# Kernel tuning notes

Measured on AMD Instinct MI355X. Metric: run time of the kernel, lower is better.

The kernel has to match this reference:

```python
import jax, jax.numpy as jnp
import numpy as np

D_MODEL = 256
N_LEVELS = 4
N_HEADS = 8
N_POINTS = 4
LEN_Q = 1024
LEN_X = 256
SHAPES_NP = np.array([[100, 100], [50, 50], [25, 25], [13, 13]], dtype=np.int32)
LEN_IN = int((SHAPES_NP[:, 0] * SHAPES_NP[:, 1]).sum())  # 13294


def setup_inputs() -> dict:
    key = jax.random.key(0)
    ks = jax.random.split(key, 10)
    s = 0.02
    lvl_start = np.concatenate([[0], np.cumsum(SHAPES_NP[:, 0] * SHAPES_NP[:, 1])[:-1]]).astype(np.int32)
    return {
        "query": jax.random.normal(ks[0], (1, LEN_Q, D_MODEL), jnp.float32),
        "reference_points": jax.random.uniform(ks[1], (1, LEN_Q, N_LEVELS, 2), jnp.float32),
        "input_flatten": jax.random.normal(ks[2], (1, LEN_IN, D_MODEL), jnp.float32),
        "input_spatial_shapes": jnp.asarray(SHAPES_NP, jnp.int32),
        "add_keys": jax.random.normal(ks[3], (1, LEN_X, D_MODEL), jnp.float32),
        "input_level_start_index": jnp.asarray(lvl_start, jnp.int32),
        "W_off": jax.random.normal(ks[4], (N_HEADS * N_LEVELS * N_POINTS * 2, D_MODEL), jnp.float32) * s,
        "b_off": jax.random.normal(ks[5], (N_HEADS * N_LEVELS * N_POINTS * 2,), jnp.float32),
        "W_attn": jax.random.normal(ks[6], (N_HEADS * (N_LEVELS + 1), D_MODEL, D_MODEL), jnp.float32) * s,
        "W_val": jax.random.normal(ks[7], (2 * N_HEADS, D_MODEL, D_MODEL), jnp.float32) * s,
        "b_val": jax.random.normal(ks[8], (2 * N_HEADS, D_MODEL), jnp.float32) * s,
        "W_mix": jax.random.normal(ks[9], (D_MODEL, N_HEADS + 1), jnp.float32) * s,
    }


def reference(query, reference_points, input_flatten, input_spatial_shapes, add_keys,
              input_level_start_index, W_off, b_off, W_attn, W_val, b_val, W_mix):
    N, Lq, C = query.shape
    H, L, P = N_HEADS, N_LEVELS, N_POINTS

    # sampling offsets: (N, Lq, H, L, P, 2)
    off = (query @ W_off.T + b_off).reshape(N, Lq, H, L, P, 2)
    iss_f = input_spatial_shapes.astype(jnp.float32)          # (L, 2) = (H_l, W_l)
    wh = iss_f[:, ::-1]                                        # (W_l, H_l)
    loc = reference_points[:, :, None, :, None, :] + off / wh[None, None, None, :, None, :]

    # get_keys: clamp, quantize to int index (matches torch .int() trunc, values >= 0)
    loc = jnp.clip(loc, 0.0, 0.999)
    idx = (loc * iss_f[None, None, None, :, None, :]).astype(jnp.int32)
    h_l = input_spatial_shapes[:, 0]                           # (L,)
    flat_idx = (idx[..., 0] + idx[..., 1] * h_l[None, None, None, :, None]
                + input_level_start_index[None, None, None, :, None])   # (N, Lq, H, L, P)
    keys = input_flatten[0][flat_idx[0]]                       # (Lq, H, L, P, C)
    keys = jnp.transpose(keys, (1, 2, 3, 0, 4))                # (H, L, P, Lq, C)

    q = query.reshape(Lq, C)
    head_w = jax.nn.softmax(W_mix.T, axis=0)                   # (H+1, C), softmax over heads
    result = q * head_w[-1][None]
    addk = add_keys.reshape(-1, C)                             # (Lx, C)

    for h in range(H):
        attn = []
        for lvl in range(L):
            simil = W_attn[h * L + lvl]
            # faithful to torch: (C, P*Lq) row-major reshaped to (P, Lq, C)
            ki = (simil @ keys[h, lvl].reshape(-1, C).T).reshape(P, Lq, C)
            attn.append((ki * q[None]).sum(-1))                # (P, Lq)
        simil = W_attn[h * L + L]
        ki = addk @ simil.T                                    # (Lx, C)
        attn.append(ki @ q.T)                                  # (Lx, Lq)
        attn = jax.nn.softmax(jnp.concatenate(attn, axis=0), axis=0)  # (L*P+Lx, Lq)

        vals = (keys[h].reshape(-1, C) @ W_val[2 * h].T + b_val[2 * h]).reshape(L * P, Lq, C)
        v2 = addk @ W_val[2 * h + 1].T + b_val[2 * h + 1]      # (Lx, C)
        vals = jnp.concatenate([vals, jnp.broadcast_to(v2[:, None], (v2.shape[0], Lq, C))], axis=0)
        result = result + (attn[:, :, None] * vals).sum(0) * head_w[h][None]

    return result[None]
```

## Files before the change

kernel.cpp:

```cpp
#include <hip/hip_runtime.h>

typedef unsigned short ushort_t;
typedef __attribute__((ext_vector_type(8))) short bh8;
typedef __attribute__((ext_vector_type(4))) float f4;
typedef __attribute__((ext_vector_type(4))) unsigned int u4;

__device__ __forceinline__ ushort_t f2bf(float f) {
  unsigned u = __float_as_uint(f);
  return (ushort_t)((u + 0x7FFFu + ((u >> 16) & 1u)) >> 16);
}
__device__ __forceinline__ float bf2f(ushort_t v) {
  return __uint_as_float(((unsigned)v) << 16);
}

template <typename OutT>
__device__ __forceinline__ void gemm_abt_core(
    char* smem,
    const ushort_t* __restrict__ A, const ushort_t* __restrict__ B,
    OutT* __restrict__ C, int ldA, int ldB, int ldC, int K, int m0, int n0)
{
  ushort_t* As = (ushort_t*)smem;
  ushort_t* Bs = (ushort_t*)(smem + 10240);
  int t = threadIdx.x;
  int lane = t & 63, w = t >> 6;
  int quad = lane >> 4, l15 = lane & 15;
  int wm = w >> 1, wn = w & 1;
  f4 acc[4][4];
  #pragma unroll
  for (int mi = 0; mi < 4; ++mi)
    #pragma unroll
    for (int ni = 0; ni < 4; ++ni) acc[mi][ni] = (f4)0.f;
  int row = t >> 1, kh = (t & 1) * 16;
  for (int k0 = 0; k0 < K; k0 += 32) {
    if (k0) __syncthreads();
    {
      const u4* ga = (const u4*)(A + (m0 + row) * ldA + k0 + kh);
      u4 v0 = ga[0], v1 = ga[1];
      u4* da = (u4*)(As + row * 40 + kh); da[0] = v0; da[1] = v1;
      const u4* gb = (const u4*)(B + (n0 + row) * ldB + k0 + kh);
      u4 u0 = gb[0], u1 = gb[1];
      u4* db = (u4*)(Bs + row * 40 + kh); db[0] = u0; db[1] = u1;
    }
    __syncthreads();
    bh8 af[4], bfv[4];
    #pragma unroll
    for (int mi = 0; mi < 4; ++mi)
      af[mi] = *(bh8*)(As + (wm * 64 + mi * 16 + l15) * 40 + quad * 8);
    #pragma unroll
    for (int ni = 0; ni < 4; ++ni)
      bfv[ni] = *(bh8*)(Bs + (wn * 64 + ni * 16 + l15) * 40 + quad * 8);
    #pragma unroll
    for (int mi = 0; mi < 4; ++mi)
      #pragma unroll
      for (int ni = 0; ni < 4; ++ni)
        acc[mi][ni] = __builtin_amdgcn_mfma_f32_16x16x32_bf16(af[mi], bfv[ni], acc[mi][ni], 0, 0, 0);
  }
  #pragma unroll
  for (int mi = 0; mi < 4; ++mi)
    #pragma unroll
    for (int ni = 0; ni < 4; ++ni)
      #pragma unroll
      for (int r = 0; r < 4; ++r) {
        int mg = m0 + wm * 64 + mi * 16 + quad * 4 + r;
        int ng = n0 + wn * 64 + ni * 16 + l15;
        if constexpr (sizeof(OutT) == 4) C[mg * ldC + ng] = acc[mi][ni][r];
        else C[mg * ldC + ng] = (OutT)f2bf(acc[mi][ni][r]);
      }
}

__global__ __launch_bounds__(256) void k_fused_cast_off(
    const float* __restrict__ q, const float* __restrict__ xin,
    const float* __restrict__ addk, const float* __restrict__ Wval,
    const float* __restrict__ Wattn, ushort_t* __restrict__ arena,
    const float* __restrict__ Woff, float* __restrict__ off_buf)
{
  if (blockIdx.x < 2048) {
    const int total4 = 1850240;
    for (int i = blockIdx.x * 256 + threadIdx.x; i < total4; i += 2048 * 256) {
      const float* src; ushort_t* dst; int e;
      if (i < 65536)        { src = q    + i * 4;            dst = arena + i * 4; }
      else if (i < 916352)  { e = i - 65536;  src = xin  + e * 4; dst = arena + 262144  + e * 4; }
      else if (i < 932736)  { e = i - 916352; src = addk + e * 4; dst = arena + 3665408 + e * 4; }
      else if (i < 1194880) {
        e = i - 932736; int el = e * 4;
        int h = el >> 17, r = el & 131071;
        int c = r >> 9, k = r & 511;
        src = Wval + (2 * h + (k >> 8)) * 65536 + c * 256 + (k & 255);
        dst = arena + 3730944 + el;
      }
      else if (i < 1325952) {
        e = i - 1194880; int el = e * 4;
        int h = el >> 16, off = el & 65535;
        src = Wattn + h * 262144 + 262144 + off;
        dst = arena + 5828096 + el;
      }
      else {
        e = i - 1325952;
        src = Wattn + e * 4;
        dst = arena + 6352384 + e * 4;
      }
      float4 v = *(const float4*)src;
      ushort4 o; o.x = f2bf(v.x); o.y = f2bf(v.y); o.z = f2bf(v.z); o.w = f2bf(v.w);
      *(ushort4*)dst = o;
    }
  } else {
    __shared__ float As[16][65];
    __shared__ float Bs[16][65];
    int e = blockIdx.x - 2048;
    int kh2 = e >> 6; e &= 63;
    int nx = e & 3, my = e >> 2;
    int m0 = my * 64, n0 = nx * 64;
    int kbase = kh2 * 128;
    int t = threadIdx.x;
    int tm = t & 15, tn = t >> 4;
    int lr = t >> 4, lc = t & 15;
    float acc[4][4] = {};
    for (int k0 = kbase; k0 < kbase + 128; k0 += 16) {
      #pragma unroll
      for (int i = 0; i < 4; ++i) {
        int r = lr + i * 16;
        As[lc][r] = q[(m0 + r) * 256 + k0 + lc];
        Bs[lc][r] = Woff[(n0 + r) * 256 + k0 + lc];
      }
      __syncthreads();
      #pragma unroll
      for (int k = 0; k < 16; ++k) {
        float a[4], b[4];
        #pragma unroll
        for (int i = 0; i < 4; ++i) a[i] = As[k][tm * 4 + i];
        #pragma unroll
        for (int j = 0; j < 4; ++j) b[j] = Bs[k][tn * 4 + j];
        #pragma unroll
        for (int i = 0; i < 4; ++i)
          #pragma unroll
          for (int j = 0; j < 4; ++j) acc[i][j] += a[i] * b[j];
      }
      __syncthreads();
    }
    #pragma unroll
    for (int i = 0; i < 4; ++i)
      #pragma unroll
      for (int j = 0; j < 4; ++j)
        off_buf[kh2 * 262144 + (m0 + tm * 4 + i) * 256 + n0 + tn * 4 + j] = acc[i][j];
  }
}

__global__ __launch_bounds__(256) void k_fused_idx_g4(
    const float* __restrict__ off_buf, const float* __restrict__ boff,
    const float* __restrict__ refpts, const int* __restrict__ shapes,
    const int* __restrict__ lvlst, int* __restrict__ fidx,
    const ushort_t* __restrict__ addk, const ushort_t* __restrict__ Wattn4,
    ushort_t* __restrict__ tmp)
{
  __shared__ __align__(16) char smem[20480];
  if (blockIdx.x < 512) {
    int t = threadIdx.x;
    int b = blockIdx.x * 2 + (t >> 7), tt = t & 127;
    int l = (tt >> 2) & 3;
    float off0 = off_buf[b * 256 + 2 * tt]     + off_buf[262144 + b * 256 + 2 * tt]     + boff[2 * tt];
    float off1 = off_buf[b * 256 + 2 * tt + 1] + off_buf[262144 + b * 256 + 2 * tt + 1] + boff[2 * tt + 1];
    int Hi = shapes[2 * l], Wi = shapes[2 * l + 1];
    float Hf = (float)Hi, Wf = (float)Wi;
    float r0 = refpts[b * 8 + 2 * l], r1 = refpts[b * 8 + 2 * l + 1];
    float l0 = fminf(fmaxf(r0 + off0 / Wf, 0.f), 0.999f);
    float l1 = fminf(fmaxf(r1 + off1 / Hf, 0.f), 0.999f);
    int i0 = (int)(l0 * Hf);
    int i1 = (int)(l1 * Wf);
    fidx[b * 128 + tt] = i0 + i1 * Hi + lvlst[l];
  } else {
    int e = blockIdx.x - 512;
    int h = e >> 2, rem = e & 3, my = rem >> 1, nx = rem & 1;
    gemm_abt_core<ushort_t>(smem, addk, Wattn4 + h * 65536, tmp + h * 65536,
                            256, 256, 256, 256, my * 128, nx * 128);
  }
}

__device__ __forceinline__ void attn_mfma_body(
    char* smemc,
    const ushort_t* __restrict__ qbf, const ushort_t* __restrict__ xbf,
    const ushort_t* __restrict__ Wlvl, const int* __restrict__ fidx,
    float* __restrict__ attnP, int bx)
{
  unsigned* Bs = (unsigned*)smemc;
  ushort_t* As = (ushort_t*)(smemc + 8704);
  int* fis = (int*)(smemc + 17920);
  float* Nlds = (float*)smemc;

  int h = bx >> 8, l = (bx >> 6) & 3, g = bx & 63;
  int ch = g & 3, g2 = g >> 2;
  int p = g2 >> 2, tg = g2 & 3;
  int c0 = ch * 64;
  int t = threadIdx.x;
  int lane = t & 63, w = t >> 6;
  int quad = lane >> 4, l15 = lane & 15;
  int qcol = p * 4 + tg;
  fis[t] = fidx[(tg * 256 + t) * 128 + h * 16 + l * 4 + p];
  __syncthreads();
  f4 acc[4];
  #pragma unroll
  for (int mi = 0; mi < 4; ++mi) acc[mi] = (f4)0.f;

  int cl = t & 63, sg = t >> 6;
  int uu = t >> 2, jj0 = (t & 3) * 16;
  const ushort_t* qrow = qbf + (uu * 16 + qcol) * 256 + jj0;

  unsigned vv[16];
  u4 a0, a1;
  #pragma unroll
  for (int rr = 0; rr < 16; ++rr)
    vv[rr] = xbf[fis[sg * 16 + rr] * 256 + c0 + cl];
  { const u4* src = (const u4*)qrow; a0 = src[0]; a1 = src[1]; }

  #pragma unroll
  for (int jt = 0; jt < 4; ++jt) {
    if (jt) __syncthreads();
    #pragma unroll
    for (int i = 0; i < 4; ++i) {
      uint2 w2; w2.x = vv[i * 4] | (vv[i * 4 + 1] << 16);
      w2.y = vv[i * 4 + 2] | (vv[i * 4 + 3] << 16);
      *(uint2*)&Bs[cl * 34 + sg * 8 + i * 2] = w2;
    }
    { u4* dst = (u4*)(As + uu * 72 + jj0); dst[0] = a0; dst[1] = a1; }
    if (jt < 3) {
      #pragma unroll
      for (int rr = 0; rr < 16; ++rr)
        vv[rr] = xbf[fis[(jt + 1) * 64 + sg * 16 + rr] * 256 + c0 + cl];
      const u4* src = (const u4*)(qrow + (jt + 1) * 64);
      a0 = src[0]; a1 = src[1];
    }
    __syncthreads();
    #pragma unroll
    for (int ks = 0; ks < 2; ++ks) {
      bh8 af[4], bfv;
      #pragma unroll
      for (int mi = 0; mi < 4; ++mi)
        af[mi] = *(bh8*)(As + (mi * 16 + l15) * 72 + ks * 32 + quad * 8);
      {
        const unsigned* bp = &Bs[(w * 16 + l15) * 34 + ks * 16 + quad * 4];
        uint2 b0 = *(const uint2*)bp;
        uint2 b1 = *(const uint2*)(bp + 2);
        u4 bb; bb.x = b0.x; bb.y = b0.y; bb.z = b1.x; bb.w = b1.y;
        bfv = __builtin_bit_cast(bh8, bb);
      }
      #pragma unroll
      for (int mi = 0; mi < 4; ++mi)
        acc[mi] = __builtin_amdgcn_mfma_f32_16x16x32_bf16(af[mi], bfv, acc[mi], 0, 0, 0);
    }
  }
  __syncthreads();
  #pragma unroll
  for (int mi = 0; mi < 4; ++mi)
    *(f4*)&Nlds[(w * 16 + l15) * 68 + mi * 16 + quad * 4] = acc[mi];
  __syncthreads();
  {
    int a = t >> 6, u = t & 63;
    const ushort_t* Wr = Wlvl + (h * 4 + l) * 65536 + (a * 64 + u) * 256 + c0;
    float s = 0.f;
    #pragma unroll
    for (int cc = 0; cc < 8; ++cc) {
      u4 wv = *(const u4*)(Wr + cc * 8);
      int cb = cc * 8;
      s += __uint_as_float(wv.x << 16)         * Nlds[(cb + 0) * 68 + u];
      s += __uint_as_float(wv.x & 0xffff0000u) * Nlds[(cb + 1) * 68 + u];
      s += __uint_as_float(wv.y << 16)         * Nlds[(cb + 2) * 68 + u];
      s += __uint_as_float(wv.y & 0xffff0000u) * Nlds[(cb + 3) * 68 + u];
      s += __uint_as_float(wv.z << 16)         * Nlds[(cb + 4) * 68 + u];
      s += __uint_as_float(wv.z & 0xffff0000u) * Nlds[(cb + 5) * 68 + u];
      s += __uint_as_float(wv.w << 16)         * Nlds[(cb + 6) * 68 + u];
      s += __uint_as_float(wv.w & 0xffff0000u) * Nlds[(cb + 7) * 68 + u];
    }
    attnP[ch * 131072 + (h * 16 + l * 4 + a) * 1024 + u * 16 + qcol] = s;
  }
}

__global__ __launch_bounds__(256) void k_fused_attn(
    const ushort_t* __restrict__ qbf, const ushort_t* __restrict__ xbf,
    const ushort_t* __restrict__ Wlvl, const int* __restrict__ fidx,
    float* __restrict__ attnP,
    const ushort_t* __restrict__ tmp, float* __restrict__ attn)
{
  __shared__ __align__(16) char smem[20480];
  int bx = blockIdx.x;
  if (bx < 2048) {
    attn_mfma_body(smem, qbf, xbf, Wlvl, fidx, attnP, bx);
  } else {
    int e = bx - 2048;
    int h = e >> 4, rem = e & 15, my = rem >> 3, nx = rem & 7;
    gemm_abt_core<float>(smem, tmp + h * 65536, qbf, attn + h * 278528 + 16384,
                         256, 256, 1024, 256, my * 128, nx * 128);
  }
}

__global__ __launch_bounds__(256) void k_softmax(
    float* __restrict__ attn, const float* __restrict__ attnP,
    ushort_t* __restrict__ attn2bf, float* __restrict__ s1, float* __restrict__ s2)
{
  __shared__ float red[8][32];
  int h = blockIdx.y;
  int b = blockIdx.x * 32 + (threadIdx.x & 31);
  int rg = threadIdx.x >> 5;
  const int R0 = rg * 34;
  float* col = attn + h * 278528 + b;
  float v[34];
  float m = -1e30f;
  #pragma unroll
  for (int i = 0; i < 34; ++i) {
    int r = R0 + i;
    float x;
    if (r < 16) {
      int idx = (h * 16 + r) * 1024 + b;
      x = attnP[idx] + attnP[131072 + idx] + attnP[262144 + idx] + attnP[393216 + idx];
    } else {
      x = col[r * 1024];
    }
    v[i] = x;
    m = fmaxf(m, x);
  }
  red[rg][threadIdx.x & 31] = m;
  __syncthreads();
  #pragma unroll
  for (int j = 0; j < 8; ++j) m = fmaxf(m, red[j][threadIdx.x & 31]);
  float sum = 0.f;
  #pragma unroll
  for (int i = 0; i < 34; ++i) { v[i] = expf(v[i] - m); sum += v[i]; }
  __syncthreads();
  red[rg][threadIdx.x & 31] = sum;
  __syncthreads();
  float tot = 0.f;
  #pragma unroll
  for (int j = 0; j < 8; ++j) tot += red[j][threadIdx.x & 31];
  float inv = 1.f / tot;
  #pragma unroll
  for (int i = 0; i < 34; ++i) {
    int r = R0 + i;
    float x = v[i] * inv;
    if (r < 16) col[r * 1024] = x;
    else attn2bf[h * 262144 + (r - 16) * 1024 + b] = f2bf(x);
  }
  if (rg == 0) {
    float sa = 0.f;
    #pragma unroll
    for (int i = 0; i < 16; ++i) sa += v[i];
    float sn = sa * inv;
    s1[h * 1024 + b] = sn;
    s2[h * 1024 + b] = 1.f - sn;
  }
}

__global__ __launch_bounds__(256) void k_fused_kbar_tn(
    const ushort_t* __restrict__ xbf, const float* __restrict__ attn,
    const int* __restrict__ fidx, const ushort_t* __restrict__ attn2,
    const ushort_t* __restrict__ addk, ushort_t* __restrict__ kabar)
{
  __shared__ __align__(16) unsigned Asu[128 * 20];
  __shared__ __align__(16) unsigned Bsu[128 * 20];
  if (blockIdx.x < 1024) {
    int h = blockIdx.x >> 7, b0 = (blockIdx.x & 127) * 8;
    int t = threadIdx.x;
    int qi = t >> 5, oct = t & 31;
    int b = b0 + qi;
    float sacc[8] = {};
    #pragma unroll
    for (int r = 0; r < 16; ++r) {
      float aw = attn[(h * 272 + r) * 1024 + b];
      int row = fidx[b * 128 + h * 16 + r];
      u4 v = *(const u4*)(xbf + row * 256 + oct * 8);
      sacc[0] += aw * __uint_as_float(v.x << 16);
      sacc[1] += aw * __uint_as_float(v.x & 0xffff0000u);
      sacc[2] += aw * __uint_as_float(v.y << 16);
      sacc[3] += aw * __uint_as_float(v.y & 0xffff0000u);
      sacc[4] += aw * __uint_as_float(v.z << 16);
      sacc[5] += aw * __uint_as_float(v.z & 0xffff0000u);
      sacc[6] += aw * __uint_as_float(v.w << 16);
      sacc[7] += aw * __uint_as_float(v.w & 0xffff0000u);
    }
    u4 o;
    o.x = (unsigned)f2bf(sacc[0]) | ((unsigned)f2bf(sacc[1]) << 16);
    o.y = (unsigned)f2bf(sacc[2]) | ((unsigned)f2bf(sacc[3]) << 16);
    o.z = (unsigned)f2bf(sacc[4]) | ((unsigned)f2bf(sacc[5]) << 16);
    o.w = (unsigned)f2bf(sacc[6]) | ((unsigned)f2bf(sacc[7]) << 16);
    *(u4*)(kabar + (h * 1024 + b) * 512 + oct * 8) = o;
  } else {
    int e = blockIdx.x - 1024;
    int h = e >> 4, rem = e & 15, my = rem >> 1, nx = rem & 1;
    const ushort_t* A = attn2 + h * 262144;
    const ushort_t* B = addk;
    ushort_t* C = kabar + h * 524288;
    int m0 = my * 128, n0 = nx * 128;
    int t = threadIdx.x;
    int lane = t & 63, w = t >> 6;
    int quad = lane >> 4, l15 = lane & 15;
    int wm = w >> 1, wn = w & 1;
    f4 acc[4][4];
    #pragma unroll
    for (int mi = 0; mi < 4; ++mi)
      #pragma unroll
      for (int ni = 0; ni < 4; ++ni) acc[mi][ni] = (f4)0.f;
    int col = t & 127, half = t >> 7;
    for (int k0 = 0; k0 < 256; k0 += 32) {
      if (k0) __syncthreads();
      #pragma unroll
      for (int i = 0; i < 4; ++i) {
        int kpp = half * 4 + i;
        int kk = k0 + kpp * 4;
        unsigned x0 = A[(kk + 0) * 1024 + m0 + col];
        unsigned x1 = A[(kk + 1) * 1024 + m0 + col];
        unsigned x2 = A[(kk + 2) * 1024 + m0 + col];
        unsigned x3 = A[(kk + 3) * 1024 + m0 + col];
        uint2 va; va.x = x0 | (x1 << 16); va.y = x2 | (x3 << 16);
        *(uint2*)&Asu[col * 20 + kpp * 2] = va;
        unsigned y0 = B[(kk + 0) * 256 + n0 + col];
        unsigned y1 = B[(kk + 1) * 256 + n0 + col];
        unsigned y2 = B[(kk + 2) * 256 + n0 + col];
        unsigned y3 = B[(kk + 3) * 256 + n0 + col];
        uint2 vb; vb.x = y0 | (y1 << 16); vb.y = y2 | (y3 << 16);
        *(uint2*)&Bsu[col * 20 + kpp * 2] = vb;
      }
      __syncthreads();
      bh8 af[4], bfv[4];
      #pragma unroll
      for (int mi = 0; mi < 4; ++mi)
        af[mi] = *(bh8*)((const ushort_t*)Asu + (wm * 64 + mi * 16 + l15) * 40 + quad * 8);
      #pragma unroll
      for (int ni = 0; ni < 4; ++ni)
        bfv[ni] = *(bh8*)((const ushort_t*)Bsu + (wn * 64 + ni * 16 + l15) * 40 + quad * 8);
      #pragma unroll
      for (int mi = 0; mi < 4; ++mi)
        #pragma unroll
        for (int ni = 0; ni < 4; ++ni)
          acc[mi][ni] = __builtin_amdgcn_mfma_f32_16x16x32_bf16(af[mi], bfv[ni], acc[mi][ni], 0, 0, 0);
    }
    #pragma unroll
    for (int mi = 0; mi < 4; ++mi)
      #pragma unroll
      for (int ni = 0; ni < 4; ++ni)
        #pragma unroll
        for (int r = 0; r < 4; ++r) {
          int mg = m0 + wm * 64 + mi * 16 + quad * 4 + r;
          int ng = n0 + wn * 64 + ni * 16 + l15;
          C[mg * 512 + 256 + ng] = f2bf(acc[mi][ni][r]);
        }
  }
}

__global__ __launch_bounds__(256) void gemm_val_k(
    const ushort_t* __restrict__ kabar, const ushort_t* __restrict__ Wcat,
    float* __restrict__ Y)
{
  __shared__ __align__(16) char smem[20480];
  int h = blockIdx.z;
  gemm_abt_core<float>(smem, kabar + h * 524288, Wcat + h * 131072, Y + h * 262144,
                       512, 512, 256, 512, blockIdx.y * 128, blockIdx.x * 128);
}

__global__ __launch_bounds__(256) void k_combine(
    const float* __restrict__ q, const float* __restrict__ Wmix,
    const float* __restrict__ Y,
    const float* __restrict__ s1, const float* __restrict__ s2,
    const float* __restrict__ bval, float* __restrict__ out)
{
  int b = blockIdx.x, c = threadIdx.x;
  float w[9];
  float m = -1e30f;
  #pragma unroll
  for (int j = 0; j < 9; ++j) { w[j] = Wmix[c * 9 + j]; m = fmaxf(m, w[j]); }
  float tot = 0.f;
  #pragma unroll
  for (int j = 0; j < 9; ++j) { w[j] = expf(w[j] - m); tot += w[j]; }
  float inv = 1.f / tot;
  float res = q[b * 256 + c] * w[8] * inv;
  #pragma unroll
  for (int hh = 0; hh < 8; ++hh) {
    float y = Y[(hh * 1024 + b) * 256 + c]
            + s1[hh * 1024 + b] * bval[(2 * hh) * 256 + c]
            + s2[hh * 1024 + b] * bval[(2 * hh + 1) * 256 + c];
    res += w[hh] * inv * y;
  }
  out[b * 256 + c] = res;
}

extern "C" void kernel_launch(void* const* d_in, const int* in_sizes, int n_in,
                              void* d_out, int out_size, void* d_ws, size_t ws_size,
                              hipStream_t stream) {
  (void)in_sizes; (void)n_in; (void)out_size; (void)ws_size;
  const float* q      = (const float*)d_in[0];
  const float* refpts = (const float*)d_in[1];
  const float* xin    = (const float*)d_in[2];
  const int*   shapes = (const int*)d_in[3];
  const float* addk   = (const float*)d_in[4];
  const int*   lvlst  = (const int*)d_in[5];
  const float* Woff   = (const float*)d_in[6];
  const float* boff   = (const float*)d_in[7];
  const float* Wattn  = (const float*)d_in[8];
  const float* Wval   = (const float*)d_in[9];
  const float* bval   = (const float*)d_in[10];
  const float* Wmix   = (const float*)d_in[11];
  float* out = (float*)d_out;
  float* ws  = (float*)d_ws;

  int*   fidx    = (int*)ws;
  float* s1      = ws + 393216;
  float* s2      = ws + 401408;
  float* attn    = ws + 409600;
  float* Y       = ws + 409600;
  ushort_t* arena = (ushort_t*)(ws + 2637824);
  ushort_t* q_bf     = arena;
  ushort_t* xin_bf   = arena + 262144;
  ushort_t* addk_bf  = arena + 3665408;
  ushort_t* Wcat_bf  = arena + 3730944;
  ushort_t* Wattn4_bf= arena + 5828096;
  ushort_t* Wlvl_bf  = arena + 6352384;
  ushort_t* tmp_bf   = arena + 8449536;
  ushort_t* attn2_bf = arena + 8973824;
  ushort_t* kabar_bf = arena + 11070976;
  float* attnP = (float*)(arena + 15265280);
  float* off_buf = (float*)(arena + 16313856);

  k_fused_cast_off<<<2176, 256, 0, stream>>>(q, xin, addk, Wval, Wattn, arena,
                                             Woff, off_buf);
  k_fused_idx_g4<<<544, 256, 0, stream>>>(off_buf, boff, refpts, shapes, lvlst,
                                          fidx, addk_bf, Wattn4_bf, tmp_bf);
  k_fused_attn<<<2176, 256, 0, stream>>>(q_bf, xin_bf, Wlvl_bf, fidx, attnP,
                                         tmp_bf, attn);
  k_softmax<<<dim3(32, 8), 256, 0, stream>>>(attn, attnP, attn2_bf, s1, s2);
  k_fused_kbar_tn<<<1152, 256, 0, stream>>>(xin_bf, attn, fidx, attn2_bf,
                                            addk_bf, kabar_bf);
  gemm_val_k<<<dim3(2, 8, 8), 256, 0, stream>>>(kabar_bf, Wcat_bf, Y);
  k_combine<<<1024, 256, 0, stream>>>(q, Wmix, Y, s1, s2, bval, out);
}
```

Measured before the change: 191.3 us.

## Register-prefetch GEMM tiles, batch gather loads, and schedule GEMM blocks first

Adds register double-buffering to the GEMM main loops: the next K-tile's global loads are issued before the barrier and compute, so load latency overlaps the MFMA/FMA work. The kbar gather kernel now loads all attention weights and indices up front and issues 16 row gathers before accumulating, which raises memory-level parallelism. The fused kernels also reorder block indices so the long-running GEMM blocks get low block IDs and start first, ahead of the elementwise blocks. The cost is higher register pressure, which may reduce occupancy.

```diff
diff --git a/kernel.cpp b/kernel.cpp
--- a/kernel.cpp
+++ b/kernel.cpp
@@ -31,15 +31,19 @@
     #pragma unroll
     for (int ni = 0; ni < 4; ++ni) acc[mi][ni] = (f4)0.f;
   int row = t >> 1, kh = (t & 1) * 16;
+  const ushort_t* pa = A + (m0 + row) * ldA + kh;
+  const ushort_t* pb = B + (n0 + row) * ldB + kh;
+  u4 va0 = *(const u4*)(pa);     u4 va1 = *(const u4*)(pa + 8);
+  u4 vb0 = *(const u4*)(pb);     u4 vb1 = *(const u4*)(pb + 8);
   for (int k0 = 0; k0 < K; k0 += 32) {
     if (k0) __syncthreads();
     {
-      const u4* ga = (const u4*)(A + (m0 + row) * ldA + k0 + kh);
-      u4 v0 = ga[0], v1 = ga[1];
-      u4* da = (u4*)(As + row * 40 + kh); da[0] = v0; da[1] = v1;
-      const u4* gb = (const u4*)(B + (n0 + row) * ldB + k0 + kh);
-      u4 u0 = gb[0], u1 = gb[1];
-      u4* db = (u4*)(Bs + row * 40 + kh); db[0] = u0; db[1] = u1;
+      u4* da = (u4*)(As + row * 40 + kh); da[0] = va0; da[1] = va1;
+      u4* db = (u4*)(Bs + row * 40 + kh); db[0] = vb0; db[1] = vb1;
+    }
+    if (k0 + 32 < K) {
+      va0 = *(const u4*)(pa + k0 + 32); va1 = *(const u4*)(pa + k0 + 40);
+      vb0 = *(const u4*)(pb + k0 + 32); vb1 = *(const u4*)(pb + k0 + 40);
     }
     __syncthreads();
     bh8 af[4], bfv[4];
@@ -74,9 +78,9 @@
     const float* __restrict__ Wattn, ushort_t* __restrict__ arena,
     const float* __restrict__ Woff, float* __restrict__ off_buf)
 {
-  if (blockIdx.x < 2048) {
+  if (blockIdx.x >= 128) {
     const int total4 = 1850240;
-    for (int i = blockIdx.x * 256 + threadIdx.x; i < total4; i += 2048 * 256) {
+    for (int i = (blockIdx.x - 128) * 256 + threadIdx.x; i < total4; i += 2048 * 256) {
       const float* src; ushort_t* dst; int e;
       if (i < 65536)        { src = q    + i * 4;            dst = arena + i * 4; }
       else if (i < 916352)  { e = i - 65536;  src = xin  + e * 4; dst = arena + 262144  + e * 4; }
@@ -106,7 +110,7 @@
   } else {
     __shared__ float As[16][65];
     __shared__ float Bs[16][65];
-    int e = blockIdx.x - 2048;
+    int e = blockIdx.x;
     int kh2 = e >> 6; e &= 63;
     int nx = e & 3, my = e >> 2;
     int m0 = my * 64, n0 = nx * 64;
@@ -115,12 +119,28 @@
     int tm = t & 15, tn = t >> 4;
     int lr = t >> 4, lc = t & 15;
     float acc[4][4] = {};
+    float qa[4], wb[4];
+    #pragma unroll
+    for (int i = 0; i < 4; ++i) {
+      int r = lr + i * 16;
+      qa[i] = q[(m0 + r) * 256 + kbase + lc];
+      wb[i] = Woff[(n0 + r) * 256 + kbase + lc];
+    }
     for (int k0 = kbase; k0 < kbase + 128; k0 += 16) {
+      if (k0 != kbase) __syncthreads();
       #pragma unroll
       for (int i = 0; i < 4; ++i) {
         int r = lr + i * 16;
-        As[lc][r] = q[(m0 + r) * 256 + k0 + lc];
-        Bs[lc][r] = Woff[(n0 + r) * 256 + k0 + lc];
+        As[lc][r] = qa[i];
+        Bs[lc][r] = wb[i];
+      }
+      if (k0 + 16 < kbase + 128) {
+        #pragma unroll
+        for (int i = 0; i < 4; ++i) {
+          int r = lr + i * 16;
+          qa[i] = q[(m0 + r) * 256 + k0 + 16 + lc];
+          wb[i] = Woff[(n0 + r) * 256 + k0 + 16 + lc];
+        }
       }
       __syncthreads();
       #pragma unroll
@@ -135,7 +155,6 @@
           #pragma unroll
           for (int j = 0; j < 4; ++j) acc[i][j] += a[i] * b[j];
       }
-      __syncthreads();
     }
     #pragma unroll
     for (int i = 0; i < 4; ++i)
@@ -153,9 +172,9 @@
     ushort_t* __restrict__ tmp)
 {
   __shared__ __align__(16) char smem[20480];
-  if (blockIdx.x < 512) {
+  if (blockIdx.x >= 32) {
     int t = threadIdx.x;
-    int b = blockIdx.x * 2 + (t >> 7), tt = t & 127;
+    int b = (blockIdx.x - 32) * 2 + (t >> 7), tt = t & 127;
     int l = (tt >> 2) & 3;
     float off0 = off_buf[b * 256 + 2 * tt]     + off_buf[262144 + b * 256 + 2 * tt]     + boff[2 * tt];
     float off1 = off_buf[b * 256 + 2 * tt + 1] + off_buf[262144 + b * 256 + 2 * tt + 1] + boff[2 * tt + 1];
@@ -168,7 +187,7 @@
     int i1 = (int)(l1 * Wf);
     fidx[b * 128 + tt] = i0 + i1 * Hi + lvlst[l];
   } else {
-    int e = blockIdx.x - 512;
+    int e = blockIdx.x;
     int h = e >> 2, rem = e & 3, my = rem >> 1, nx = rem & 1;
     gemm_abt_core<ushort_t>(smem, addk, Wattn4 + h * 65536, tmp + h * 65536,
                             256, 256, 256, 256, my * 128, nx * 128);
@@ -281,10 +300,10 @@
 {
   __shared__ __align__(16) char smem[20480];
   int bx = blockIdx.x;
-  if (bx < 2048) {
-    attn_mfma_body(smem, qbf, xbf, Wlvl, fidx, attnP, bx);
+  if (bx >= 128) {
+    attn_mfma_body(smem, qbf, xbf, Wlvl, fidx, attnP, bx - 128);
   } else {
-    int e = bx - 2048;
+    int e = bx;
     int h = e >> 4, rem = e & 15, my = rem >> 3, nx = rem & 7;
     gemm_abt_core<float>(smem, tmp + h * 65536, qbf, attn + h * 278528 + 16384,
                          256, 256, 1024, 256, my * 128, nx * 128);
@@ -354,25 +373,47 @@
 {
   __shared__ __align__(16) unsigned Asu[128 * 20];
   __shared__ __align__(16) unsigned Bsu[128 * 20];
-  if (blockIdx.x < 1024) {
-    int h = blockIdx.x >> 7, b0 = (blockIdx.x & 127) * 8;
+  if (blockIdx.x >= 128) {
+    int bb = blockIdx.x - 128;
+    int h = bb >> 7, b0 = (bb & 127) * 8;
     int t = threadIdx.x;
     int qi = t >> 5, oct = t & 31;
     int b = b0 + qi;
+    float aw[16]; int rowv[16];
+    #pragma unroll
+    for (int r = 0; r < 16; ++r) {
+      aw[r]   = attn[(h * 272 + r) * 1024 + b];
+      rowv[r] = fidx[b * 128 + h * 16 + r];
+    }
+    u4 va[8], vb[8];
+    #pragma unroll
+    for (int r = 0; r < 8; ++r) va[r] = *(const u4*)(xbf + rowv[r] * 256 + oct * 8);
+    #pragma unroll
+    for (int r = 0; r < 8; ++r) vb[r] = *(const u4*)(xbf + rowv[8 + r] * 256 + oct * 8);
     float sacc[8] = {};
     #pragma unroll
-    for (int r = 0; r < 16; ++r) {
-      float aw = attn[(h * 272 + r) * 1024 + b];
-      int row = fidx[b * 128 + h * 16 + r];
-      u4 v = *(const u4*)(xbf + row * 256 + oct * 8);
-      sacc[0] += aw * __uint_as_float(v.x << 16);
-      sacc[1] += aw * __uint_as_float(v.x & 0xffff0000u);
-      sacc[2] += aw * __uint_as_float(v.y << 16);
-      sacc[3] += aw * __uint_as_float(v.y & 0xffff0000u);
-      sacc[4] += aw * __uint_as_float(v.z << 16);
-      sacc[5] += aw * __uint_as_float(v.z & 0xffff0000u);
-      sacc[6] += aw * __uint_as_float(v.w << 16);
-      sacc[7] += aw * __uint_as_float(v.w & 0xffff0000u);
+    for (int r = 0; r < 8; ++r) {
+      u4 v = va[r]; float w = aw[r];
+      sacc[0] += w * __uint_as_float(v.x << 16);
+      sacc[1] += w * __uint_as_float(v.x & 0xffff0000u);
+      sacc[2] += w * __uint_as_float(v.y << 16);
+      sacc[3] += w * __uint_as_float(v.y & 0xffff0000u);
+      sacc[4] += w * __uint_as_float(v.z << 16);
+      sacc[5] += w * __uint_as_float(v.z & 0xffff0000u);
+      sacc[6] += w * __uint_as_float(v.w << 16);
+      sacc[7] += w * __uint_as_float(v.w & 0xffff0000u);
+    }
+    #pragma unroll
+    for (int r = 0; r < 8; ++r) {
+      u4 v = vb[r]; float w = aw[8 + r];
+      sacc[0] += w * __uint_as_float(v.x << 16);
+      sacc[1] += w * __uint_as_float(v.x & 0xffff0000u);
+      sacc[2] += w * __uint_as_float(v.y << 16);
+      sacc[3] += w * __uint_as_float(v.y & 0xffff0000u);
+      sacc[4] += w * __uint_as_float(v.z << 16);
+      sacc[5] += w * __uint_as_float(v.z & 0xffff0000u);
+      sacc[6] += w * __uint_as_float(v.w << 16);
+      sacc[7] += w * __uint_as_float(v.w & 0xffff0000u);
     }
     u4 o;
     o.x = (unsigned)f2bf(sacc[0]) | ((unsigned)f2bf(sacc[1]) << 16);
@@ -381,7 +422,7 @@
     o.w = (unsigned)f2bf(sacc[6]) | ((unsigned)f2bf(sacc[7]) << 16);
     *(u4*)(kabar + (h * 1024 + b) * 512 + oct * 8) = o;
   } else {
-    int e = blockIdx.x - 1024;
+    int e = blockIdx.x;
     int h = e >> 4, rem = e & 15, my = rem >> 1, nx = rem & 1;
     const ushort_t* A = attn2 + h * 262144;
     const ushort_t* B = addk;
@@ -397,24 +438,38 @@
       #pragma unroll
       for (int ni = 0; ni < 4; ++ni) acc[mi][ni] = (f4)0.f;
     int col = t & 127, half = t >> 7;
+    unsigned pa[8], pb[8];
+    #pragma unroll
+    for (int i = 0; i < 4; ++i) {
+      int kpp = half * 4 + i, kk = kpp * 4;
+      unsigned x0 = A[(kk + 0) * 1024 + m0 + col], x1 = A[(kk + 1) * 1024 + m0 + col];
+      unsigned x2 = A[(kk + 2) * 1024 + m0 + col], x3 = A[(kk + 3) * 1024 + m0 + col];
+      pa[i * 2] = x0 | (x1 << 16); pa[i * 2 + 1] = x2 | (x3 << 16);
+      unsigned y0 = B[(kk + 0) * 256 + n0 + col], y1 = B[(kk + 1) * 256 + n0 + col];
+      unsigned y2 = B[(kk + 2) * 256 + n0 + col], y3 = B[(kk + 3) * 256 + n0 + col];
+      pb[i * 2] = y0 | (y1 << 16); pb[i * 2 + 1] = y2 | (y3 << 16);
+    }
     for (int k0 = 0; k0 < 256; k0 += 32) {
       if (k0) __syncthreads();
       #pragma unroll
       for (int i = 0; i < 4; ++i) {
         int kpp = half * 4 + i;
-        int kk = k0 + kpp * 4;
-        unsigned x0 = A[(kk + 0) * 1024 + m0 + col];
-        unsigned x1 = A[(kk + 1) * 1024 + m0 + col];
-        unsigned x2 = A[(kk + 2) * 1024 + m0 + col];
-        unsigned x3 = A[(kk + 3) * 1024 + m0 + col];
-        uint2 va; va.x = x0 | (x1 << 16); va.y = x2 | (x3 << 16);
+        uint2 va; va.x = pa[i * 2]; va.y = pa[i * 2 + 1];
         *(uint2*)&Asu[col * 20 + kpp * 2] = va;
-        unsigned y0 = B[(kk + 0) * 256 + n0 + col];
-        unsigned y1 = B[(kk + 1) * 256 + n0 + col];
-        unsigned y2 = B[(kk + 2) * 256 + n0 + col];
-        unsigned y3 = B[(kk + 3) * 256 + n0 + col];
-        uint2 vb; vb.x = y0 | (y1 << 16); vb.y = y2 | (y3 << 16);
-        *(uint2*)&Bsu[col * 20 + kpp * 2] = vb;
+        uint2 vbv; vbv.x = pb[i * 2]; vbv.y = pb[i * 2 + 1];
+        *(uint2*)&Bsu[col * 20 + kpp * 2] = vbv;
+      }
+      if (k0 + 32 < 256) {
+        #pragma unroll
+        for (int i = 0; i < 4; ++i) {
+          int kpp = half * 4 + i, kk = k0 + 32 + kpp * 4;
+          unsigned x0 = A[(kk + 0) * 1024 + m0 + col], x1 = A[(kk + 1) * 1024 + m0 + col];
+          unsigned x2 = A[(kk + 2) * 1024 + m0 + col], x3 = A[(kk + 3) * 1024 + m0 + col];
+          pa[i * 2] = x0 | (x1 << 16); pa[i * 2 + 1] = x2 | (x3 << 16);
+          unsigned y0 = B[(kk + 0) * 256 + n0 + col], y1 = B[(kk + 1) * 256 + n0 + col];
+          unsigned y2 = B[(kk + 2) * 256 + n0 + col], y3 = B[(kk + 3) * 256 + n0 + col];
+          pb[i * 2] = y0 | (y1 << 16); pb[i * 2 + 1] = y2 | (y3 << 16);
+        }
       }
       __syncthreads();
       bh8 af[4], bfv[4];
```

After: 177.0 us. 1.08x faster.
